# Kernel optimization log

Measured on AMD Instinct MI355X. Metric: run time of the kernel, lower is better.

## Reference

```python
import jax, jax.numpy as jnp
import numpy as np

N = 20480      # total nodes
E = 327680     # total edges (avg degree 16)
B = 16         # graphs in batch
IN = 16        # node feature dim
H = 8          # hidden_out_channel
CO = 64        # conv_out_channel
ET = 36        # n_edge_types
EF = 2         # edge_features
OUT = 1        # classifier out
DIMS = [(IN, H), (H, H), (H, H), (H, CO)]


def setup_inputs() -> dict:
    key = jax.random.key(0)
    ks = jax.random.split(key, 32)
    inp = {}
    inp['x'] = jax.random.normal(ks[0], (N, IN), jnp.float32)
    inp['edge_index'] = jax.random.randint(ks[1], (2, E), 0, N)
    inp['edge_type'] = jax.random.randint(ks[2], (E,), 0, ET)
    inp['edge_attr'] = jax.random.normal(ks[3], (E, EF), jnp.float32)
    inp['cell_type'] = jax.random.randint(ks[4], (N,), 0, 2)
    inp['batch'] = (jnp.arange(N) // (N // B)).astype(jnp.int32)
    i = 5
    for l, (ci, co) in enumerate(DIMS, 1):
        d = ci * co
        s = 1.0 / np.sqrt(EF)
        inp[f'emb{l}'] = jax.random.normal(ks[i], (ET, d), jnp.float32) * 0.02; i += 1
        inp[f'wh{l}'] = jax.random.normal(ks[i], (EF, d), jnp.float32) * s; i += 1
        inp[f'bh{l}'] = jnp.zeros((d,), jnp.float32)
        inp[f'wg{l}'] = jax.random.normal(ks[i], (EF, d), jnp.float32) * s; i += 1
        inp[f'bg{l}'] = jnp.zeros((d,), jnp.float32)
        inp[f'root{l}'] = jax.random.normal(ks[i], (ci, co), jnp.float32) / np.sqrt(ci); i += 1
        inp[f'bias{l}'] = jnp.zeros((co,), jnp.float32)
    inp['clf_w'] = jax.random.normal(ks[i], (CO, OUT), jnp.float32) / np.sqrt(CO)
    inp['clf_b'] = jnp.zeros((OUT,), jnp.float32)
    return inp


def edge_weights(etype, ef, emb, wh, bh, wg, bg):
    # EdgeNN: relu(embedding(type) * fc_h(feat) + fc_g(feat)) -> [E, cin*cout]
    return jax.nn.relu(emb[etype] * (ef @ wh + bh) + (ef @ wg + bg))


def nnconv(h, src, dst, W, root, bias):
    # NNConv(aggr='mean', root_weight=True): gather src feats, per-edge matmul, scatter-mean
    cin, cout = root.shape
    msg = jnp.einsum('ei,eio->eo', h[src], W.reshape(-1, cin, cout))  # [E, cout]
    agg = jax.ops.segment_sum(msg, dst, num_segments=N)
    deg = jax.ops.segment_sum(jnp.ones_like(msg[:, 0]), dst, num_segments=N)
    return agg / jnp.maximum(deg, 1.0)[:, None] + h @ root + bias


def reference(x, edge_index, edge_type, edge_attr, cell_type, batch,
              emb1, wh1, bh1, wg1, bg1, root1, bias1,
              emb2, wh2, bh2, wg2, bg2, root2, bias2,
              emb3, wh3, bh3, wg3, bg3, root3, bias3,
              emb4, wh4, bh4, wg4, bg4, root4, bias4,
              clf_w, clf_b):
    src, dst = edge_index[0], edge_index[1]
    layers = [(emb1, wh1, bh1, wg1, bg1, root1, bias1),
              (emb2, wh2, bh2, wg2, bg2, root2, bias2),
              (emb3, wh3, bh3, wg3, bg3, root3, bias3),
              (emb4, wh4, bh4, wg4, bg4, root4, bias4)]
    h = x
    for (emb, wh, bh, wg, bg, root, bias) in layers:  # fixed 4 structurally-distinct layers
        W = edge_weights(edge_type, edge_attr, emb, wh, bh, wg, bg)
        h = jax.nn.relu(nnconv(h, src, dst, W, root, bias))
    # gated scatter-mean pooling over tumor cells (cell_type == 1)
    gate = (cell_type == 1).astype(jnp.int32)
    seg = gate * (batch.astype(jnp.int32) + 1)  # 0 = masked-out bucket
    pooled = jax.ops.segment_sum(h, seg, num_segments=B + 1)
    cnt = jax.ops.segment_sum(jnp.ones((h.shape[0],), h.dtype), seg, num_segments=B + 1)
    pooled = (pooled / jnp.maximum(cnt, 1.0)[:, None])[1:B + 1]  # [B, CO]
    return jax.nn.sigmoid(pooled @ clf_w + clf_b)  # hazards [B, OUT]
```

## Files before the change

kernel.cpp:

```cpp
#include <hip/hip_runtime.h>
#include <math.h>

#define NN 20480
#define NE 327680
#define NBATCH 16

typedef float v2f __attribute__((ext_vector_type(2)));

static __device__ __forceinline__ v2f vmax0(v2f a) {
  v2f r; r.x = fmaxf(a.x, 0.f); r.y = fmaxf(a.y, 0.f); return r;
}
#define VMAX0 vmax0

__global__ __launch_bounds__(256) void prep_kernel(
    const int* __restrict__ dst, int* __restrict__ cnt,
    const float* __restrict__ e4, float* __restrict__ t4) {
  int b = blockIdx.x;
  if (b < NE / 256) {
    int e = b * 256 + threadIdx.x;
    atomicAdd(&cnt[dst[e]], 1);
  } else {
    int idx = (b - NE / 256) * 256 + threadIdx.x;
    int t = idx >> 9, r = idx & 511, o = r >> 3, i = r & 7;
    t4[idx] = e4[(t << 9) + i * 64 + o];
  }
}

__global__ __launch_bounds__(1024) void scan_kernel(const int* __restrict__ cnt,
                                                    int* __restrict__ off,
                                                    int* __restrict__ cur,
                                                    float* __restrict__ poolz) {
  __shared__ int part[1024];
  int tid = threadIdx.x;
  if (tid < NBATCH * 64 + NBATCH) poolz[tid] = 0.f;
  const int PT = NN / 1024;
  int loc[PT];
  int run = 0;
  int base = tid * PT;
#pragma unroll
  for (int k = 0; k < PT; k++) { loc[k] = run; run += cnt[base + k]; }
  part[tid] = run;
  __syncthreads();
  for (int d = 1; d < 1024; d <<= 1) {
    int t = (tid >= d) ? part[tid - d] : 0;
    __syncthreads();
    part[tid] += t;
    __syncthreads();
  }
  int pre = (tid == 0) ? 0 : part[tid - 1];
#pragma unroll
  for (int k = 0; k < PT; k++) {
    off[base + k] = pre + loc[k];
    cur[base + k] = pre + loc[k];
  }
  if (tid == 1023) off[NN] = pre + run;
}

__global__ void scatter_kernel(const int* __restrict__ src, const int* __restrict__ dst,
                               const int* __restrict__ etype, const float* __restrict__ eattr,
                               int* __restrict__ cur, float4* __restrict__ es) {
  int e = blockIdx.x * blockDim.x + threadIdx.x;
  if (e >= NE) return;
  int d = dst[e];
  int pos = atomicAdd(&cur[d], 1);
  es[pos] = make_float4(__int_as_float(src[e]), __int_as_float(etype[e]),
                        eattr[2 * e], eattr[2 * e + 1]);
}

__global__ __launch_bounds__(256) void layer_small16(
    const int* __restrict__ off, const float4* __restrict__ es,
    const float* __restrict__ h_in,
    const float* __restrict__ emb, const float* __restrict__ wh,
    const float* __restrict__ bh, const float* __restrict__ wg,
    const float* __restrict__ bg,
    const float* __restrict__ root, const float* __restrict__ bias,
    float* __restrict__ h_out) {
  constexpr int D = 128;
  constexpr int S = D + 1;
  __shared__ float semb[36 * S];
  for (int idx = threadIdx.x; idx < 36 * D; idx += 256) {
    int t = idx / D, io = idx - t * D;
    semb[t * S + io] = emb[idx];
  }
  int lane = threadIdx.x & 63;
  int o = lane & 7;
  int ihalf = (lane >> 3) & 1;
  int esub = lane >> 4;
  int ibase = ihalf * 8;
  v2f rwh0[4], rwh1[4], rbh[4], rwg0[4], rwg1[4], rbg[4], rroot[4];
#pragma unroll
  for (int p = 0; p < 4; p++) {
    int a = (ibase + 2 * p) * 8 + o, b = (ibase + 2 * p + 1) * 8 + o;
    rwh0[p] = (v2f){wh[a], wh[b]};
    rwh1[p] = (v2f){wh[D + a], wh[D + b]};
    rbh[p]  = (v2f){bh[a], bh[b]};
    rwg0[p] = (v2f){wg[a], wg[b]};
    rwg1[p] = (v2f){wg[D + a], wg[D + b]};
    rbg[p]  = (v2f){bg[a], bg[b]};
    rroot[p] = (v2f){root[a], root[b]};
  }
  float rbias = bias[o];
  __syncthreads();
  int wid = __builtin_amdgcn_readfirstlane(blockIdx.x * 4 + (threadIdx.x >> 6));
  for (int k = 0; k < 2; k++) {
    int n = wid * 2 + k;
    int beg = off[n], end = off[n + 1];
    float acc = 0.f;
    for (int j = beg + esub; j < end; j += 4) {
      float4 rec = es[j];
      int s = __float_as_int(rec.x);
      int t = __float_as_int(rec.y);
      v2f ef0 = (v2f){rec.z, rec.z}, ef1 = (v2f){rec.w, rec.w};
      const float4* hp = (const float4*)(h_in + s * 16 + ibase);
      float4 h0 = hp[0], h1 = hp[1];
      v2f hv[4] = {(v2f){h0.x, h0.y}, (v2f){h0.z, h0.w},
                   (v2f){h1.x, h1.y}, (v2f){h1.z, h1.w}};
      const float* st = &semb[t * S + ibase * 8 + o];
      v2f msg = {0.f, 0.f};
#pragma unroll
      for (int p = 0; p < 4; p++) {
        v2f hval = ef0 * rwh0[p] + ef1 * rwh1[p] + rbh[p];
        v2f gval = ef0 * rwg0[p] + ef1 * rwg1[p] + rbg[p];
        v2f stv = (v2f){st[(2 * p) * 8], st[(2 * p + 1) * 8]};
        msg += hv[p] * VMAX0(stv * hval + gval);
      }
      acc += msg.x + msg.y;
    }
    acc += __shfl_xor(acc, 8);
    acc += __shfl_xor(acc, 16);
    acc += __shfl_xor(acc, 32);
    const float* hn = h_in + n * 16 + ibase;
    v2f rtv = {0.f, 0.f};
#pragma unroll
    for (int p = 0; p < 4; p++)
      rtv += (v2f){hn[2 * p], hn[2 * p + 1]} * rroot[p];
    float rt = rtv.x + rtv.y;
    rt += __shfl_xor(rt, 8);
    float deg = (float)(end - beg);
    float val = fmaxf(rbias + rt + acc / fmaxf(deg, 1.f), 0.f);
    if (lane < 8) h_out[n * 8 + o] = val;
  }
}

__global__ __launch_bounds__(256) void layer_small8(
    const int* __restrict__ off, const float4* __restrict__ es,
    const float* __restrict__ h_in,
    const float* __restrict__ emb, const float* __restrict__ wh,
    const float* __restrict__ bh, const float* __restrict__ wg,
    const float* __restrict__ bg,
    const float* __restrict__ root, const float* __restrict__ bias,
    float* __restrict__ h_out) {
  constexpr int D = 64;
  constexpr int S = D + 1;
  __shared__ float semb[36 * S];
  for (int idx = threadIdx.x; idx < 36 * D; idx += 256) {
    int t = idx / D, io = idx - t * D;
    semb[t * S + io] = emb[idx];
  }
  int lane = threadIdx.x & 63;
  int o = lane & 7, esub = lane >> 3;
  v2f rwh0[4], rwh1[4], rbh[4], rwg0[4], rwg1[4], rbg[4], rroot[4];
#pragma unroll
  for (int p = 0; p < 4; p++) {
    int a = (2 * p) * 8 + o, b = (2 * p + 1) * 8 + o;
    rwh0[p] = (v2f){wh[a], wh[b]};
    rwh1[p] = (v2f){wh[D + a], wh[D + b]};
    rbh[p]  = (v2f){bh[a], bh[b]};
    rwg0[p] = (v2f){wg[a], wg[b]};
    rwg1[p] = (v2f){wg[D + a], wg[D + b]};
    rbg[p]  = (v2f){bg[a], bg[b]};
    rroot[p] = (v2f){root[a], root[b]};
  }
  float rbias = bias[o];
  __syncthreads();
  int wid = __builtin_amdgcn_readfirstlane(blockIdx.x * 4 + (threadIdx.x >> 6));
  for (int k = 0; k < 4; k++) {
    int n = wid * 4 + k;
    int beg = off[n], end = off[n + 1];
    float acc = 0.f;
    for (int j = beg + esub; j < end; j += 8) {
      float4 rec = es[j];
      int s = __float_as_int(rec.x);
      int t = __float_as_int(rec.y);
      v2f ef0 = (v2f){rec.z, rec.z}, ef1 = (v2f){rec.w, rec.w};
      const float4* hp = (const float4*)(h_in + s * 8);
      float4 h0 = hp[0], h1 = hp[1];
      v2f hv[4] = {(v2f){h0.x, h0.y}, (v2f){h0.z, h0.w},
                   (v2f){h1.x, h1.y}, (v2f){h1.z, h1.w}};
      const float* st = &semb[t * S + o];
      v2f msg = {0.f, 0.f};
#pragma unroll
      for (int p = 0; p < 4; p++) {
        v2f hval = ef0 * rwh0[p] + ef1 * rwh1[p] + rbh[p];
        v2f gval = ef0 * rwg0[p] + ef1 * rwg1[p] + rbg[p];
        v2f stv = (v2f){st[(2 * p) * 8], st[(2 * p + 1) * 8]};
        msg += hv[p] * VMAX0(stv * hval + gval);
      }
      acc += msg.x + msg.y;
    }
    acc += __shfl_xor(acc, 8);
    acc += __shfl_xor(acc, 16);
    acc += __shfl_xor(acc, 32);
    float deg = (float)(end - beg);
    const float* hn = h_in + n * 8;
    v2f rtv = {0.f, 0.f};
#pragma unroll
    for (int p = 0; p < 4; p++)
      rtv += (v2f){hn[2 * p], hn[2 * p + 1]} * rroot[p];
    float val = fmaxf(rbias + rtv.x + rtv.y + acc / fmaxf(deg, 1.f), 0.f);
    if (lane < 8) h_out[n * 8 + o] = val;
  }
}

__global__ __launch_bounds__(256) void layer_l4(
    const int* __restrict__ off, const float4* __restrict__ es,
    const float* __restrict__ h_in, const float* __restrict__ embT,
    const float* __restrict__ wh, const float* __restrict__ bh,
    const float* __restrict__ wg, const float* __restrict__ bg,
    const float* __restrict__ root, const float* __restrict__ bias,
    float* __restrict__ h_out) {
  int lane = threadIdx.x & 63;
  v2f rwh0[4], rwh1[4], rbh[4], rwg0[4], rwg1[4], rbg[4], rroot[4];
#pragma unroll
  for (int p = 0; p < 4; p++) {
    int a = (2 * p) * 64 + lane, b = (2 * p + 1) * 64 + lane;
    rwh0[p] = (v2f){wh[a], wh[b]};
    rwh1[p] = (v2f){wh[512 + a], wh[512 + b]};
    rbh[p]  = (v2f){bh[a], bh[b]};
    rwg0[p] = (v2f){wg[a], wg[b]};
    rwg1[p] = (v2f){wg[512 + a], wg[512 + b]};
    rbg[p]  = (v2f){bg[a], bg[b]};
    rroot[p] = (v2f){root[a], root[b]};
  }
  float rbias = bias[lane];
  int n = __builtin_amdgcn_readfirstlane((int)(blockIdx.x * 4) + (int)(threadIdx.x >> 6));
  int beg = off[n], end = off[n + 1];
  float acc0 = 0.f, acc1 = 0.f;
  int e = beg;
  for (; e + 2 <= end; e += 2) {
    float4 r0 = es[e], r1 = es[e + 1];
    int s0 = __float_as_int(r0.x), t0 = __float_as_int(r0.y);
    int s1 = __float_as_int(r1.x), t1 = __float_as_int(r1.y);
    const float4* hp0 = (const float4*)(h_in + s0 * 8);
    const float4* hp1 = (const float4*)(h_in + s1 * 8);
    float4 a0 = hp0[0], a1 = hp0[1];
    float4 b0 = hp1[0], b1 = hp1[1];
    const float4* ep0 = (const float4*)(embT + t0 * 512 + lane * 8);
    const float4* ep1 = (const float4*)(embT + t1 * 512 + lane * 8);
    float4 s00 = ep0[0], s01 = ep0[1];
    float4 s10 = ep1[0], s11 = ep1[1];
    v2f sv0[4] = {(v2f){s00.x, s00.y}, (v2f){s00.z, s00.w},
                  (v2f){s01.x, s01.y}, (v2f){s01.z, s01.w}};
    v2f sv1[4] = {(v2f){s10.x, s10.y}, (v2f){s10.z, s10.w},
                  (v2f){s11.x, s11.y}, (v2f){s11.z, s11.w}};
    v2f hva[4] = {(v2f){a0.x, a0.y}, (v2f){a0.z, a0.w},
                  (v2f){a1.x, a1.y}, (v2f){a1.z, a1.w}};
    v2f hvb[4] = {(v2f){b0.x, b0.y}, (v2f){b0.z, b0.w},
                  (v2f){b1.x, b1.y}, (v2f){b1.z, b1.w}};
    v2f e00 = (v2f){r0.z, r0.z}, e01 = (v2f){r0.w, r0.w};
    v2f e10 = (v2f){r1.z, r1.z}, e11 = (v2f){r1.w, r1.w};
    v2f m0 = {0.f, 0.f}, m1 = {0.f, 0.f};
#pragma unroll
    for (int p = 0; p < 4; p++) {
      v2f hv0 = e00 * rwh0[p] + e01 * rwh1[p] + rbh[p];
      v2f gv0 = e00 * rwg0[p] + e01 * rwg1[p] + rbg[p];
      m0 += hva[p] * VMAX0(sv0[p] * hv0 + gv0);
      v2f hv1 = e10 * rwh0[p] + e11 * rwh1[p] + rbh[p];
      v2f gv1 = e10 * rwg0[p] + e11 * rwg1[p] + rbg[p];
      m1 += hvb[p] * VMAX0(sv1[p] * hv1 + gv1);
    }
    acc0 += m0.x + m0.y;
    acc1 += m1.x + m1.y;
  }
  if (e < end) {
    float4 r0 = es[e];
    int s0 = __float_as_int(r0.x), t0 = __float_as_int(r0.y);
    const float4* hp0 = (const float4*)(h_in + s0 * 8);
    float4 a0 = hp0[0], a1 = hp0[1];
    const float4* ep0 = (const float4*)(embT + t0 * 512 + lane * 8);
    float4 s00 = ep0[0], s01 = ep0[1];
    v2f sv0[4] = {(v2f){s00.x, s00.y}, (v2f){s00.z, s00.w},
                  (v2f){s01.x, s01.y}, (v2f){s01.z, s01.w}};
    v2f hva[4] = {(v2f){a0.x, a0.y}, (v2f){a0.z, a0.w},
                  (v2f){a1.x, a1.y}, (v2f){a1.z, a1.w}};
    v2f e00 = (v2f){r0.z, r0.z}, e01 = (v2f){r0.w, r0.w};
    v2f m0 = {0.f, 0.f};
#pragma unroll
    for (int p = 0; p < 4; p++) {
      v2f hv0 = e00 * rwh0[p] + e01 * rwh1[p] + rbh[p];
      v2f gv0 = e00 * rwg0[p] + e01 * rwg1[p] + rbg[p];
      m0 += hva[p] * VMAX0(sv0[p] * hv0 + gv0);
    }
    acc0 += m0.x + m0.y;
  }
  float acc = acc0 + acc1;
  float deg = (float)(end - beg);
  const float* hn = h_in + n * 8;
  v2f rtv = {0.f, 0.f};
#pragma unroll
  for (int p = 0; p < 4; p++)
    rtv += (v2f){hn[2 * p], hn[2 * p + 1]} * rroot[p];
  h_out[n * 64 + lane] = fmaxf(rbias + rtv.x + rtv.y + acc / fmaxf(deg, 1.f), 0.f);
}

__global__ __launch_bounds__(256) void pool1_kernel(
    const float* __restrict__ h4, const int* __restrict__ ct,
    float* __restrict__ pooled, float* __restrict__ pcnt) {
  __shared__ float ss[4][64];
  __shared__ float sc[4];
  int b = blockIdx.x / 20, c = blockIdx.x % 20;
  int base = b * (NN / NBATCH) + c * 64;
  int o = threadIdx.x & 63, sub = threadIdx.x >> 6;
  float sum = 0.f, cnt = 0.f;
  for (int j = sub; j < 64; j += 4) {
    int n = base + j;
    if (ct[n] == 1) { sum += h4[n * 64 + o]; cnt += 1.f; }
  }
  ss[sub][o] = sum;
  if (o == 0) sc[sub] = cnt;
  __syncthreads();
  if (threadIdx.x < 64) {
    float tot = ss[0][o] + ss[1][o] + ss[2][o] + ss[3][o];
    unsafeAtomicAdd(&pooled[b * 64 + o], tot);
    if (o == 0) unsafeAtomicAdd(&pcnt[b], sc[0] + sc[1] + sc[2] + sc[3]);
  }
}

__global__ __launch_bounds__(1024) void pool2_kernel(
    const float* __restrict__ pooled, const float* __restrict__ pcnt,
    const float* __restrict__ clf_w, const float* __restrict__ clf_b,
    float* __restrict__ out) {
  int b = threadIdx.x >> 6, o = threadIdx.x & 63;
  float c = pcnt[b];
  float v = (pooled[b * 64 + o] / fmaxf(c, 1.f)) * clf_w[o];
#pragma unroll
  for (int d = 32; d; d >>= 1) v += __shfl_down(v, d);
  if (o == 0) out[b] = 1.f / (1.f + expf(-(v + clf_b[0])));
}

extern "C" void kernel_launch(void* const* d_in, const int* in_sizes, int n_in,
                              void* d_out, int out_size, void* d_ws, size_t ws_size,
                              hipStream_t stream) {
  (void)in_sizes; (void)n_in; (void)out_size; (void)ws_size;
  const float* x     = (const float*)d_in[0];
  const int*   eidx  = (const int*)d_in[1];
  const int*   src   = eidx;
  const int*   dst   = eidx + NE;
  const int*   etype = (const int*)d_in[2];
  const float* eattr = (const float*)d_in[3];
  const int*   ct    = (const int*)d_in[4];
  const float *emb[4], *wh[4], *bh[4], *wg[4], *bg[4], *root[4], *bias[4];
  for (int l = 0; l < 4; l++) {
    int b0 = 6 + 7 * l;
    emb[l]  = (const float*)d_in[b0 + 0];
    wh[l]   = (const float*)d_in[b0 + 1];
    bh[l]   = (const float*)d_in[b0 + 2];
    wg[l]   = (const float*)d_in[b0 + 3];
    bg[l]   = (const float*)d_in[b0 + 4];
    root[l] = (const float*)d_in[b0 + 5];
    bias[l] = (const float*)d_in[b0 + 6];
  }
  const float* clf_w = (const float*)d_in[34];
  const float* clf_b = (const float*)d_in[35];
  float* outp = (float*)d_out;

  float* ws  = (float*)d_ws;
  int*    off    = (int*)ws;
  float4* es     = (float4*)(ws + 20484);
  float*  hA     = ws + 20484 + 4 * NE;
  float*  hB     = hA + 8 * NN;
  float*  h4     = hB + 8 * NN;
  float*  embT4  = h4 + 64 * NN;
  float*  pooled = embT4 + 36 * 512;
  float*  pcnt   = pooled + 16 * 64;
  int*    cnt    = (int*)h4;
  int*    cur    = cnt + NN;

  hipMemsetAsync(cnt, 0, NN * sizeof(int), stream);
  prep_kernel<<<NE / 256 + 72, 256, 0, stream>>>(dst, cnt, emb[3], embT4);
  scan_kernel<<<1, 1024, 0, stream>>>(cnt, off, cur, pooled);
  scatter_kernel<<<NE / 256, 256, 0, stream>>>(src, dst, etype, eattr, cur, es);

  layer_small16<<<2560, 256, 0, stream>>>(off, es, x,
      emb[0], wh[0], bh[0], wg[0], bg[0], root[0], bias[0], hA);
  layer_small8<<<1280, 256, 0, stream>>>(off, es, hA,
      emb[1], wh[1], bh[1], wg[1], bg[1], root[1], bias[1], hB);
  layer_small8<<<1280, 256, 0, stream>>>(off, es, hB,
      emb[2], wh[2], bh[2], wg[2], bg[2], root[2], bias[2], hA);
  layer_l4<<<NN / 4, 256, 0, stream>>>(off, es, hA, embT4,
      wh[3], bh[3], wg[3], bg[3], root[3], bias[3], h4);

  pool1_kernel<<<320, 256, 0, stream>>>(h4, ct, pooled, pcnt);
  pool2_kernel<<<1, 1024, 0, stream>>>(pooled, pcnt, clf_w, clf_b, outp);
}
```

Measured before the change: 294.6 us.

## Stage layer-4 edge-type embedding in LDS and process multiple nodes per wave

```diff
diff --git a/kernel.cpp b/kernel.cpp
--- a/kernel.cpp
+++ b/kernel.cpp
@@ -21,8 +21,9 @@
     atomicAdd(&cnt[dst[e]], 1);
   } else {
     int idx = (b - NE / 256) * 256 + threadIdx.x;
-    int t = idx >> 9, r = idx & 511, o = r >> 3, i = r & 7;
-    t4[idx] = e4[(t << 9) + i * 64 + o];
+    int t = idx >> 9, rem = idx & 511;
+    int q = rem >> 7, o = (rem >> 1) & 63, r = rem & 1;
+    t4[idx] = e4[(t << 9) + (((q << 1) | r) << 6) + o];
   }
 }
 
@@ -119,8 +120,8 @@
       v2f msg = {0.f, 0.f};
 #pragma unroll
       for (int p = 0; p < 4; p++) {
-        v2f hval = ef0 * rwh0[p] + ef1 * rwh1[p] + rbh[p];
-        v2f gval = ef0 * rwg0[p] + ef1 * rwg1[p] + rbg[p];
+        v2f hval = rbh[p] + ef0 * rwh0[p] + ef1 * rwh1[p];
+        v2f gval = rbg[p] + ef0 * rwg0[p] + ef1 * rwg1[p];
         v2f stv = (v2f){st[(2 * p) * 8], st[(2 * p + 1) * 8]};
         msg += hv[p] * VMAX0(stv * hval + gval);
       }
@@ -191,8 +192,8 @@
       v2f msg = {0.f, 0.f};
 #pragma unroll
       for (int p = 0; p < 4; p++) {
-        v2f hval = ef0 * rwh0[p] + ef1 * rwh1[p] + rbh[p];
-        v2f gval = ef0 * rwg0[p] + ef1 * rwg1[p] + rbg[p];
+        v2f hval = rbh[p] + ef0 * rwh0[p] + ef1 * rwh1[p];
+        v2f gval = rbg[p] + ef0 * rwg0[p] + ef1 * rwg1[p];
         v2f stv = (v2f){st[(2 * p) * 8], st[(2 * p + 1) * 8]};
         msg += hv[p] * VMAX0(stv * hval + gval);
       }
@@ -212,13 +213,16 @@
   }
 }
 
-__global__ __launch_bounds__(256) void layer_l4(
+__global__ __launch_bounds__(512) void layer_l4(
     const int* __restrict__ off, const float4* __restrict__ es,
     const float* __restrict__ h_in, const float* __restrict__ embT,
     const float* __restrict__ wh, const float* __restrict__ bh,
     const float* __restrict__ wg, const float* __restrict__ bg,
     const float* __restrict__ root, const float* __restrict__ bias,
     float* __restrict__ h_out) {
+  __shared__ float semb[36 * 512];
+  for (int idx = threadIdx.x; idx < 36 * 128; idx += 512)
+    ((float4*)semb)[idx] = ((const float4*)embT)[idx];
   int lane = threadIdx.x & 63;
   v2f rwh0[4], rwh1[4], rbh[4], rwg0[4], rwg1[4], rbg[4], rroot[4];
 #pragma unroll
@@ -233,74 +237,80 @@
     rroot[p] = (v2f){root[a], root[b]};
   }
   float rbias = bias[lane];
-  int n = __builtin_amdgcn_readfirstlane((int)(blockIdx.x * 4) + (int)(threadIdx.x >> 6));
-  int beg = off[n], end = off[n + 1];
-  float acc0 = 0.f, acc1 = 0.f;
-  int e = beg;
-  for (; e + 2 <= end; e += 2) {
-    float4 r0 = es[e], r1 = es[e + 1];
-    int s0 = __float_as_int(r0.x), t0 = __float_as_int(r0.y);
-    int s1 = __float_as_int(r1.x), t1 = __float_as_int(r1.y);
-    const float4* hp0 = (const float4*)(h_in + s0 * 8);
-    const float4* hp1 = (const float4*)(h_in + s1 * 8);
-    float4 a0 = hp0[0], a1 = hp0[1];
-    float4 b0 = hp1[0], b1 = hp1[1];
-    const float4* ep0 = (const float4*)(embT + t0 * 512 + lane * 8);
-    const float4* ep1 = (const float4*)(embT + t1 * 512 + lane * 8);
-    float4 s00 = ep0[0], s01 = ep0[1];
-    float4 s10 = ep1[0], s11 = ep1[1];
-    v2f sv0[4] = {(v2f){s00.x, s00.y}, (v2f){s00.z, s00.w},
-                  (v2f){s01.x, s01.y}, (v2f){s01.z, s01.w}};
-    v2f sv1[4] = {(v2f){s10.x, s10.y}, (v2f){s10.z, s10.w},
-                  (v2f){s11.x, s11.y}, (v2f){s11.z, s11.w}};
-    v2f hva[4] = {(v2f){a0.x, a0.y}, (v2f){a0.z, a0.w},
-                  (v2f){a1.x, a1.y}, (v2f){a1.z, a1.w}};
-    v2f hvb[4] = {(v2f){b0.x, b0.y}, (v2f){b0.z, b0.w},
-                  (v2f){b1.x, b1.y}, (v2f){b1.z, b1.w}};
-    v2f e00 = (v2f){r0.z, r0.z}, e01 = (v2f){r0.w, r0.w};
-    v2f e10 = (v2f){r1.z, r1.z}, e11 = (v2f){r1.w, r1.w};
-    v2f m0 = {0.f, 0.f}, m1 = {0.f, 0.f};
-#pragma unroll
-    for (int p = 0; p < 4; p++) {
-      v2f hv0 = e00 * rwh0[p] + e01 * rwh1[p] + rbh[p];
-      v2f gv0 = e00 * rwg0[p] + e01 * rwg1[p] + rbg[p];
-      m0 += hva[p] * VMAX0(sv0[p] * hv0 + gv0);
-      v2f hv1 = e10 * rwh0[p] + e11 * rwh1[p] + rbh[p];
-      v2f gv1 = e10 * rwg0[p] + e11 * rwg1[p] + rbg[p];
-      m1 += hvb[p] * VMAX0(sv1[p] * hv1 + gv1);
+  __syncthreads();
+  int base = __builtin_amdgcn_readfirstlane(
+      (int)(blockIdx.x * 40) + (int)(threadIdx.x >> 6) * 5);
+  const float* sl = &semb[lane * 2];
+  for (int k = 0; k < 5; k++) {
+    int n = base + k;
+    int beg = off[n], end = off[n + 1];
+    float acc0 = 0.f, acc1 = 0.f;
+    int e = beg;
+    for (; e + 2 <= end; e += 2) {
+      float4 r0 = es[e], r1 = es[e + 1];
+      int s0 = __float_as_int(r0.x), t0 = __float_as_int(r0.y);
+      int s1 = __float_as_int(r1.x), t1 = __float_as_int(r1.y);
+      const float4* hp0 = (const float4*)(h_in + s0 * 8);
+      const float4* hp1 = (const float4*)(h_in + s1 * 8);
+      float4 a0 = hp0[0], a1 = hp0[1];
+      float4 b0 = hp1[0], b1 = hp1[1];
+      const float* st0 = sl + t0 * 512;
+      const float* st1 = sl + t1 * 512;
+      v2f sv0[4], sv1[4];
+#pragma unroll
+      for (int q = 0; q < 4; q++) {
+        sv0[q] = *(const v2f*)(st0 + q * 128);
+        sv1[q] = *(const v2f*)(st1 + q * 128);
+      }
+      v2f hva[4] = {(v2f){a0.x, a0.y}, (v2f){a0.z, a0.w},
+                    (v2f){a1.x, a1.y}, (v2f){a1.z, a1.w}};
+      v2f hvb[4] = {(v2f){b0.x, b0.y}, (v2f){b0.z, b0.w},
+                    (v2f){b1.x, b1.y}, (v2f){b1.z, b1.w}};
+      v2f e00 = (v2f){r0.z, r0.z}, e01 = (v2f){r0.w, r0.w};
+      v2f e10 = (v2f){r1.z, r1.z}, e11 = (v2f){r1.w, r1.w};
+      v2f m0 = {0.f, 0.f}, m1 = {0.f, 0.f};
+#pragma unroll
+      for (int p = 0; p < 4; p++) {
+        v2f hv0 = rbh[p] + e00 * rwh0[p] + e01 * rwh1[p];
+        v2f gv0 = rbg[p] + e00 * rwg0[p] + e01 * rwg1[p];
+        m0 += hva[p] * VMAX0(sv0[p] * hv0 + gv0);
+        v2f hv1 = rbh[p] + e10 * rwh0[p] + e11 * rwh1[p];
+        v2f gv1 = rbg[p] + e10 * rwg0[p] + e11 * rwg1[p];
+        m1 += hvb[p] * VMAX0(sv1[p] * hv1 + gv1);
+      }
+      acc0 += m0.x + m0.y;
+      acc1 += m1.x + m1.y;
     }
-    acc0 += m0.x + m0.y;
-    acc1 += m1.x + m1.y;
-  }
-  if (e < end) {
-    float4 r0 = es[e];
-    int s0 = __float_as_int(r0.x), t0 = __float_as_int(r0.y);
-    const float4* hp0 = (const float4*)(h_in + s0 * 8);
-    float4 a0 = hp0[0], a1 = hp0[1];
-    const float4* ep0 = (const float4*)(embT + t0 * 512 + lane * 8);
-    float4 s00 = ep0[0], s01 = ep0[1];
-    v2f sv0[4] = {(v2f){s00.x, s00.y}, (v2f){s00.z, s00.w},
-                  (v2f){s01.x, s01.y}, (v2f){s01.z, s01.w}};
-    v2f hva[4] = {(v2f){a0.x, a0.y}, (v2f){a0.z, a0.w},
-                  (v2f){a1.x, a1.y}, (v2f){a1.z, a1.w}};
-    v2f e00 = (v2f){r0.z, r0.z}, e01 = (v2f){r0.w, r0.w};
-    v2f m0 = {0.f, 0.f};
-#pragma unroll
-    for (int p = 0; p < 4; p++) {
-      v2f hv0 = e00 * rwh0[p] + e01 * rwh1[p] + rbh[p];
-      v2f gv0 = e00 * rwg0[p] + e01 * rwg1[p] + rbg[p];
-      m0 += hva[p] * VMAX0(sv0[p] * hv0 + gv0);
+    if (e < end) {
+      float4 r0 = es[e];
+      int s0 = __float_as_int(r0.x), t0 = __float_as_int(r0.y);
+      const float4* hp0 = (const float4*)(h_in + s0 * 8);
+      float4 a0 = hp0[0], a1 = hp0[1];
+      const float* st0 = sl + t0 * 512;
+      v2f sv0[4];
+#pragma unroll
+      for (int q = 0; q < 4; q++) sv0[q] = *(const v2f*)(st0 + q * 128);
+      v2f hva[4] = {(v2f){a0.x, a0.y}, (v2f){a0.z, a0.w},
+                    (v2f){a1.x, a1.y}, (v2f){a1.z, a1.w}};
+      v2f e00 = (v2f){r0.z, r0.z}, e01 = (v2f){r0.w, r0.w};
+      v2f m0 = {0.f, 0.f};
+#pragma unroll
+      for (int p = 0; p < 4; p++) {
+        v2f hv0 = rbh[p] + e00 * rwh0[p] + e01 * rwh1[p];
+        v2f gv0 = rbg[p] + e00 * rwg0[p] + e01 * rwg1[p];
+        m0 += hva[p] * VMAX0(sv0[p] * hv0 + gv0);
+      }
+      acc0 += m0.x + m0.y;
     }
-    acc0 += m0.x + m0.y;
-  }
-  float acc = acc0 + acc1;
-  float deg = (float)(end - beg);
-  const float* hn = h_in + n * 8;
-  v2f rtv = {0.f, 0.f};
-#pragma unroll
-  for (int p = 0; p < 4; p++)
-    rtv += (v2f){hn[2 * p], hn[2 * p + 1]} * rroot[p];
-  h_out[n * 64 + lane] = fmaxf(rbias + rtv.x + rtv.y + acc / fmaxf(deg, 1.f), 0.f);
+    float acc = acc0 + acc1;
+    float deg = (float)(end - beg);
+    const float* hn = h_in + n * 8;
+    v2f rtv = {0.f, 0.f};
+#pragma unroll
+    for (int p = 0; p < 4; p++)
+      rtv += (v2f){hn[2 * p], hn[2 * p + 1]} * rroot[p];
+    h_out[n * 64 + lane] = fmaxf(rbias + rtv.x + rtv.y + acc / fmaxf(deg, 1.f), 0.f);
+  }
 }
 
 __global__ __launch_bounds__(256) void pool1_kernel(
@@ -387,7 +397,7 @@
       emb[1], wh[1], bh[1], wg[1], bg[1], root[1], bias[1], hB);
   layer_small8<<<1280, 256, 0, stream>>>(off, es, hB,
       emb[2], wh[2], bh[2], wg[2], bg[2], root[2], bias[2], hA);
-  layer_l4<<<NN / 4, 256, 0, stream>>>(off, es, hA, embT4,
+  layer_l4<<<NN / 40, 512, 0, stream>>>(off, es, hA, embT4,
       wh[3], bh[3], wg[3], bg[3], root[3], bias[3], h4);
 
   pool1_kernel<<<320, 256, 0, stream>>>(h4, ct, pooled, pcnt);
```

After: 292.4 us. About the same (-0.8%).
